# Optimization experiments

Hardware: AMD Instinct MI355X
Metric: run time of the kernel (lower is better)

The kernel has to match this reference:

```python
import jax, jax.numpy as jnp
import numpy as np

N_EMB = 1024
N_HEADS = 16
HS = N_EMB // N_HEADS  # 64
BASE = 10000.0


def _rope_cache(T):
    # theta uses dim = n_emb (as in the source), sliced to hs//2 frequencies
    i = jnp.arange(HS // 2, dtype=jnp.float32)
    theta = BASE ** (-2.0 * i / N_EMB)            # [hs/2]
    pos = jnp.arange(T, dtype=jnp.float32)        # [T]
    ang = pos[:, None] * theta[None, :]           # [T, hs/2]
    return jnp.cos(ang), jnp.sin(ang)


def _apply_rope(x, cos, sin):
    # x: [B, T, nh, hs]; rotate consecutive pairs along hs
    b, t, nh, hs = x.shape
    xr = x.reshape(b, t, nh, hs // 2, 2)
    c = cos[None, :, None, :]
    s = sin[None, :, None, :]
    r0 = xr[..., 0] * c - xr[..., 1] * s
    r1 = xr[..., 1] * c + xr[..., 0] * s
    return jnp.stack([r0, r1], axis=-1).reshape(b, t, nh, hs)


def setup_inputs() -> dict:
    key = jax.random.key(0)
    k1, k2, k3, k4 = jax.random.split(key, 4)
    B, T = 2, 2048
    w_std = 0.02
    x = jax.random.normal(k1, (B, T, N_EMB), jnp.float32)
    Wq = jax.random.normal(k2, (N_EMB, N_EMB), jnp.float32) * w_std
    Wk = jax.random.normal(k3, (N_EMB, N_EMB), jnp.float32) * w_std
    Wv = jax.random.normal(k4, (N_EMB, N_EMB), jnp.float32) * w_std
    return {"x": x, "Wq": Wq, "Wk": Wk, "Wv": Wv}


def reference(x, Wq, Wk, Wv):
    B, T, C = x.shape
    # nn.Linear(bias=False): y = x @ W.T
    q = (x @ Wq.T).reshape(B, T, N_HEADS, HS)
    k = (x @ Wk.T).reshape(B, T, N_HEADS, HS)
    v = (x @ Wv.T).reshape(B, T, N_HEADS, HS)
    cos, sin = _rope_cache(T)
    q = _apply_rope(q, cos, sin)
    k = _apply_rope(k, cos, sin)
    # scale uses C (n_emb), as in the source (not head_size)
    wei = jnp.einsum('bqhd,bkhd->bhqk', q, k) * (C ** -0.5)  # [B, nh, T, T]
    mask = jnp.tril(jnp.ones((T, T), dtype=bool))
    wei = jnp.where(mask[None, None], wei, -jnp.inf)
    wei = jax.nn.softmax(wei, axis=-1)
    # dropout is identity in eval mode
    out = jnp.einsum('bhqk,bkhd->bqhd', wei, v).reshape(B, T, C)
    return out
```

## Files before the change

kernel.cpp:

```cpp
#include <hip/hip_runtime.h>
#include <stdint.h>

typedef unsigned short u16;
typedef __bf16 bf16x8 __attribute__((ext_vector_type(8)));
typedef unsigned short u16x8 __attribute__((ext_vector_type(8)));
typedef unsigned short u16x4 __attribute__((ext_vector_type(4)));
typedef float f32x4 __attribute__((ext_vector_type(4)));
typedef uint32_t u32v4 __attribute__((ext_vector_type(4)));

#define LOG2E 1.4426950408889634f

typedef const __attribute__((address_space(1))) uint32_t as1_u32;
typedef __attribute__((address_space(3))) uint32_t as3_u32;

__device__ __forceinline__ u16 f2bf(float f) {
  union { float f; uint32_t i; } v; v.f = f;
  uint32_t r = (v.i + 0x7fffu + ((v.i >> 16) & 1u)) >> 16;
  return (u16)r;
}
__device__ __forceinline__ float bf2f(u16 u) {
  union { uint32_t i; float f; } v; v.i = ((uint32_t)u) << 16; return v.f;
}

__device__ __forceinline__ void gld_lds16(const void* g, void* l) {
  as1_u32* gp = (as1_u32*)((uintptr_t)g);
  as3_u32* lp = (as3_u32*)(uint32_t)(uintptr_t)(l);
  __builtin_amdgcn_global_load_lds(gp, lp, 16, 0, 0);
}

__device__ __forceinline__ float fast_exp2(float x) {
  float r;
  asm("v_exp_f32 %0, %1" : "=v"(r) : "v"(x));
  return r;
}

__global__ __launch_bounds__(256) void f32_to_bf16(
    const float* __restrict__ x, const float* __restrict__ wq,
    const float* __restrict__ wk, const float* __restrict__ wv,
    u16* __restrict__ xc, u16* __restrict__ wqc,
    u16* __restrict__ wkc, u16* __restrict__ wvc) {
  const int z = blockIdx.y;
  const float* src = z == 0 ? x : (z == 1 ? wq : (z == 2 ? wk : wv));
  u16* dst = z == 0 ? xc : (z == 1 ? wqc : (z == 2 ? wkc : wvc));
  const int n = z == 0 ? (1 << 22) : (1 << 20);

  const int idx = (blockIdx.x * 256 + (int)threadIdx.x) * 8;
  if (idx >= n) return;
  const f32x4 a = *(const f32x4*)&src[idx];
  const f32x4 b = *(const f32x4*)&src[idx + 4];
  u16x8 o;
#pragma unroll
  for (int j = 0; j < 4; j++) { o[j] = f2bf(a[j]); o[j + 4] = f2bf(b[j]); }
  *(u16x8*)&dst[idx] = o;
}

__global__ __launch_bounds__(256) void qkv_gemm(
    const u16* __restrict__ xc, const u16* __restrict__ wqc,
    const u16* __restrict__ wkc, const u16* __restrict__ wvc,
    u16* __restrict__ qo, u16* __restrict__ ko, u16* __restrict__ vt) {
  __shared__ __align__(16) u16 As[128 * 64];
  __shared__ __align__(16) u16 Bs[128 * 64];

  const int tid = threadIdx.x;
  const int lane = tid & 63;
  const int w = tid >> 6;
  const int wm = w >> 1, wn = w & 1;
  const int quad = lane >> 4, m16 = lane & 15;
  const int which = blockIdx.z;

  const u16* __restrict__ Ap;
  const u16* __restrict__ Bp;
  int m0, n0;
  if (which == 2) {
    Ap = wvc; Bp = xc;
    m0 = blockIdx.x * 128;
    n0 = blockIdx.y * 128;
  } else {
    Ap = xc; Bp = which == 0 ? wqc : wkc;
    m0 = blockIdx.y * 128;
    n0 = blockIdx.x * 128;
  }

  const f32x4 z4 = {0.f, 0.f, 0.f, 0.f};
  f32x4 acc[4][4];
#pragma unroll
  for (int i = 0; i < 4; i++)
#pragma unroll
    for (int j = 0; j < 4; j++) acc[i][j] = z4;

  const int lrow = lane >> 3;
  const int scol = ((lane & 7) ^ (lrow & 7)) * 8;
  const int srowA = m0 + w * 32 + lrow;
  const int srowB = n0 + w * 32 + lrow;
  const int rsw = m16 & 7;

  for (int k0 = 0; k0 < 1024; k0 += 64) {
    __syncthreads();
#pragma unroll
    for (int j = 0; j < 4; j++) {
      gld_lds16(&Ap[(size_t)(srowA + j * 8) * 1024 + k0 + scol],
                &As[(w * 32 + j * 8) * 64]);
      gld_lds16(&Bp[(size_t)(srowB + j * 8) * 1024 + k0 + scol],
                &Bs[(w * 32 + j * 8) * 64]);
    }
    __syncthreads();

#pragma unroll
    for (int kk = 0; kk < 2; kk++) {
      bf16x8 af[4], bfr[4];
      const int csw = ((kk * 4) ^ rsw) * 8;
#pragma unroll
      for (int t = 0; t < 4; t++) {
        af[t] = *(const bf16x8*)
            &As[(wm * 64 + t * 16 + m16) * 64 + (((kk * 4 + quad) ^ rsw) * 8)];
        bfr[t] = *(const bf16x8*)
            &Bs[(wn * 64 + t * 16 + m16) * 64 + (((kk * 4 + quad) ^ rsw) * 8)];
      }
      (void)csw;
#pragma unroll
      for (int mt = 0; mt < 4; mt++)
#pragma unroll
        for (int nt = 0; nt < 4; nt++)
          acc[mt][nt] = __builtin_amdgcn_mfma_f32_16x16x32_bf16(
              af[mt], bfr[nt], acc[mt][nt], 0, 0, 0);
    }
  }

  if (which < 2) {
    u16* __restrict__ out = which == 0 ? qo : ko;
#pragma unroll
    for (int mt = 0; mt < 4; mt++) {
      const int row = m0 + wm * 64 + mt * 16 + quad * 4;
#pragma unroll
      for (int nt = 0; nt < 4; nt++) {
        const int n = n0 + wn * 64 + nt * 16 + m16;
        f32x4 a = acc[mt][nt];
#pragma unroll
        for (int r = 0; r < 4; r++)
          out[(size_t)(row + r) * 1024 + n] = f2bf(a[r]);
      }
    }
  } else {
    const int m16p = (m16 & 3) | ((m16 & 4) << 1) | ((m16 & 8) >> 1);
#pragma unroll
    for (int mt = 0; mt < 4; mt++) {
      const int row = m0 + wm * 64 + mt * 16 + quad * 4;
#pragma unroll
      for (int nt = 0; nt < 4; nt++) {
        const int n = n0 + wn * 64 + nt * 16 + m16p;
        f32x4 a = acc[mt][nt];
#pragma unroll
        for (int r = 0; r < 4; r++)
          vt[(size_t)(row + r) * 4096 + n] = f2bf(a[r]);
      }
    }
  }
}

__global__ __launch_bounds__(256) void rope_inplace(u16* __restrict__ qb,
                                                    u16* __restrict__ kb) {
  u16* buf = blockIdx.y == 0 ? qb : kb;
  const int p = blockIdx.x * 256 + (int)threadIdx.x;
  const int e0 = p * 8;
  const int row = e0 >> 10;
  const int col0 = e0 & 1023;
  const int t = row & 2047;
  const float tf = (float)t;

  u16x8 d = *(const u16x8*)&buf[(size_t)row * 1024 + col0];
  u16x8 o;
#pragma unroll
  for (int j = 0; j < 4; j++) {
    const int i = ((col0 & 63) >> 1) + j;
    const float th = fast_exp2(-(float)i * 0.02595256324130752f);
    const float rev = tf * th * 0.15915494309189535f;
    float fr, s, c;
    asm("v_fract_f32 %0, %1" : "=v"(fr) : "v"(rev));
    asm("v_sin_f32 %0, %1" : "=v"(s) : "v"(fr));
    asm("v_cos_f32 %0, %1" : "=v"(c) : "v"(fr));
    const float a0 = bf2f(d[2 * j]), a1 = bf2f(d[2 * j + 1]);
    o[2 * j]     = f2bf(a0 * c - a1 * s);
    o[2 * j + 1] = f2bf(a1 * c + a0 * s);
  }
  *(u16x8*)&buf[(size_t)row * 1024 + col0] = o;
}

__global__ __launch_bounds__(256, 4) void flash_attn(
    const u16* __restrict__ qg, const u16* __restrict__ kg,
    const u16* __restrict__ vt, float* __restrict__ out) {
  __shared__ __align__(16) u16 Ks[128 * 72];
  __shared__ __align__(16) u16 Vs[64 * 136];

  const int tid = threadIdx.x, lane = tid & 63, w = tid >> 6;
  const int quad = lane >> 4, m16 = lane & 15;

  const int id   = (int)blockIdx.x;
  const int X    = id & 7;
  const int rem  = id >> 3;
  const int qt   = 31 - (rem >> 2);
  const int vloc = rem & 3;
  const int v    = X * 4 + vloc;
  const int h    = v & 15;
  const int b    = v >> 4;

  const size_t base  = (size_t)b * 2048 * 1024 + (size_t)h * 64;
  const size_t vbase = (size_t)(h * 64) * 4096 + (size_t)b * 2048;
  const float SC = 0.03125f * LOG2E;
  const f32x4 z4 = {0.f, 0.f, 0.f, 0.f};
  const int srow = tid >> 2, sc = (tid & 3) * 16;

  union { u16x8 u; bf16x8 f; } ones;
#pragma unroll
  for (int k = 0; k < 8; k++) ones.u[k] = 0x3F80;

  const int q0 = qt * 64;
  const int nr = (qt + 2) >> 1;

  const u16* qsrc = &qg[base + (size_t)(q0 + w * 16 + m16) * 1024 + quad * 8];
  const bf16x8 qf0 = *(const bf16x8*)qsrc;
  const bf16x8 qf1 = *(const bf16x8*)(qsrc + 32);

  u16x8 kr0, kr1, kr2, kr3, vr0, vr1, vr2, vr3;
  {
    const u16* ks = &kg[base + (size_t)srow * 1024 + sc];
    kr0 = *(const u16x8*)ks; kr1 = *(const u16x8*)(ks + 8);
    const u16* ks2 = ks + (size_t)64 * 1024;
    kr2 = *(const u16x8*)ks2; kr3 = *(const u16x8*)(ks2 + 8);
    const u16* vs = &vt[vbase + (size_t)srow * 4096 + sc];
    vr0 = *(const u16x8*)vs; vr1 = *(const u16x8*)(vs + 8);
    vr2 = *(const u16x8*)(vs + 64); vr3 = *(const u16x8*)(vs + 72);
  }

  f32x4 l4 = z4;
  f32x4 O[4];
#pragma unroll
  for (int d = 0; d < 4; d++) O[d] = z4;

  const int qrow0 = q0 + w * 16 + quad * 4;
  const int qcol  = q0 + w * 16 + m16;

  for (int rr = 0; rr < nr; ++rr) {
    const int k0 = rr * 128;
    if (rr) __syncthreads();
    *(u16x8*)&Ks[srow * 72 + sc] = kr0;
    *(u16x8*)&Ks[srow * 72 + sc + 8] = kr1;
    *(u16x8*)&Ks[(64 + srow) * 72 + sc] = kr2;
    *(u16x8*)&Ks[(64 + srow) * 72 + sc + 8] = kr3;
    *(u16x8*)&Vs[srow * 136 + sc] = vr0;
    *(u16x8*)&Vs[srow * 136 + sc + 8] = vr1;
    *(u16x8*)&Vs[srow * 136 + 64 + sc] = vr2;
    *(u16x8*)&Vs[srow * 136 + 64 + sc + 8] = vr3;
    __syncthreads();
    if (rr + 1 < nr) {
      const u16* ks = &kg[base + (size_t)(k0 + 128 + srow) * 1024 + sc];
      kr0 = *(const u16x8*)ks; kr1 = *(const u16x8*)(ks + 8);
      const u16* ks2 = ks + (size_t)64 * 1024;
      kr2 = *(const u16x8*)ks2; kr3 = *(const u16x8*)(ks2 + 8);
      const u16* vs = &vt[vbase + (size_t)srow * 4096 + k0 + 128 + sc];
      vr0 = *(const u16x8*)vs; vr1 = *(const u16x8*)(vs + 8);
      vr2 = *(const u16x8*)(vs + 64); vr3 = *(const u16x8*)(vs + 72);
    }

    f32x4 S[8];
#pragma unroll
    for (int nt = 0; nt < 8; nt++) {
      const bf16x8 kf0 = *(const bf16x8*)&Ks[(nt * 16 + m16) * 72 + quad * 8];
      const bf16x8 kf1 =
          *(const bf16x8*)&Ks[(nt * 16 + m16) * 72 + 32 + quad * 8];
      S[nt] = __builtin_amdgcn_mfma_f32_16x16x32_bf16(kf0, qf0, z4, 0, 0, 0);
      S[nt] = __builtin_amdgcn_mfma_f32_16x16x32_bf16(kf1, qf1, S[nt], 0, 0, 0);
    }

    const bool lastr = (rr == nr - 1);
    uint32_t W[16];
#pragma unroll
    for (int nt = 0; nt < 8; nt++) {
      float p[4];
#pragma unroll
      for (int r = 0; r < 4; r++) {
        float e = fast_exp2(S[nt][r] * SC);
        const int key = k0 + nt * 16 + quad * 4 + r;
        if (lastr && key > qcol) e = 0.f;
        p[r] = e;
      }
      uint32_t w0, w1;
      asm("v_cvt_pk_bf16_f32 %0, %1, %2" : "=v"(w0) : "v"(p[0]), "v"(p[1]));
      asm("v_cvt_pk_bf16_f32 %0, %1, %2" : "=v"(w1) : "v"(p[2]), "v"(p[3]));
      W[2 * nt] = w0; W[2 * nt + 1] = w1;
    }

    union { u32v4 u; bf16x8 f; } P[4];
#pragma unroll
    for (int ks = 0; ks < 4; ks++) {
      uint32_t a0 = W[4 * ks], b0 = W[4 * ks + 2];
      uint32_t a1 = W[4 * ks + 1], b1 = W[4 * ks + 3];
      asm("v_permlane32_swap_b32 %0, %1" : "+v"(a0), "+v"(b0));
      asm("v_permlane32_swap_b32 %0, %1" : "+v"(a1), "+v"(b1));
      P[ks].u = (u32v4){a0, a1, b0, b1};
    }

#pragma unroll
    for (int ks = 0; ks < 4; ks++)
      l4 = __builtin_amdgcn_mfma_f32_16x16x32_bf16(P[ks].f, ones.f, l4,
                                                   0, 0, 0);

#pragma unroll
    for (int dt = 0; dt < 4; dt++) {
#pragma unroll
      for (int ks = 0; ks < 4; ks++) {
        const bf16x8 vf =
            *(const bf16x8*)&Vs[(dt * 16 + m16) * 136 + ks * 32 + quad * 8];
        O[dt] = __builtin_amdgcn_mfma_f32_16x16x32_bf16(P[ks].f, vf, O[dt],
                                                        0, 0, 0);
      }
    }
  }

  float inv[4];
#pragma unroll
  for (int r = 0; r < 4; r++) inv[r] = 1.0f / l4[r];

#pragma unroll
  for (int dt = 0; dt < 4; dt++)
#pragma unroll
    for (int r = 0; r < 4; r++)
      out[base + (size_t)(qrow0 + r) * 1024 + dt * 16 + m16] =
          O[dt][r] * inv[r];
}

extern "C" void kernel_launch(void* const* d_in, const int* in_sizes, int n_in,
                              void* d_out, int out_size, void* d_ws, size_t ws_size,
                              hipStream_t stream) {
  const float* x  = (const float*)d_in[0];
  const float* Wq = (const float*)d_in[1];
  const float* Wk = (const float*)d_in[2];
  const float* Wv = (const float*)d_in[3];
  u16* qb  = (u16*)d_ws;
  u16* kb  = qb  + (size_t)4096 * 1024;
  u16* vtw = kb  + (size_t)4096 * 1024;
  u16* xc  = vtw + (size_t)4096 * 1024;
  u16* wqc = xc  + (size_t)4096 * 1024;
  u16* wkc = wqc + (size_t)1024 * 1024;
  u16* wvc = wkc + (size_t)1024 * 1024;

  f32_to_bf16<<<dim3(2048, 4), 256, 0, stream>>>(x, Wq, Wk, Wv,
                                                 xc, wqc, wkc, wvc);
  qkv_gemm<<<dim3(8, 32, 3), 256, 0, stream>>>(xc, wqc, wkc, wvc,
                                               qb, kb, vtw);
  rope_inplace<<<dim3(2048, 2), 256, 0, stream>>>(qb, kb);
  flash_attn<<<dim3(1024, 1, 1), 256, 0, stream>>>(qb, kb, vtw, (float*)d_out);
}
```

Before: 153.5 us.

## Fuse RoPE into QKV GEMM epilogue and process 128-row query tiles in attention

RoPE is now applied in the Q/K GEMM epilogue, rotating each pair with a lane-xor shuffle, so the separate in-place rope kernel and its extra read/write of Q and K are gone. The flash attention kernel now gives each wave two 16-row query groups (128 query rows per block). Each K/V tile loaded into LDS is reused twice as often, and the grid shrinks to 512 blocks with paired light/heavy causal tiles to balance load. The cost is higher register pressure, with launch bounds dropped to 2 blocks per SM, which lowers occupancy.

After: 162.0 us. +5.5%, slower.

```diff
diff --git a/kernel.cpp b/kernel.cpp
--- a/kernel.cpp
+++ b/kernel.cpp
@@ -4,7 +4,6 @@
 typedef unsigned short u16;
 typedef __bf16 bf16x8 __attribute__((ext_vector_type(8)));
 typedef unsigned short u16x8 __attribute__((ext_vector_type(8)));
-typedef unsigned short u16x4 __attribute__((ext_vector_type(4)));
 typedef float f32x4 __attribute__((ext_vector_type(4)));
 typedef uint32_t u32v4 __attribute__((ext_vector_type(4)));
 
@@ -108,7 +107,6 @@
 #pragma unroll
     for (int kk = 0; kk < 2; kk++) {
       bf16x8 af[4], bfr[4];
-      const int csw = ((kk * 4) ^ rsw) * 8;
 #pragma unroll
       for (int t = 0; t < 4; t++) {
         af[t] = *(const bf16x8*)
@@ -116,7 +114,6 @@
         bfr[t] = *(const bf16x8*)
             &Bs[(wn * 64 + t * 16 + m16) * 64 + (((kk * 4 + quad) ^ rsw) * 8)];
       }
-      (void)csw;
 #pragma unroll
       for (int mt = 0; mt < 4; mt++)
 #pragma unroll
@@ -128,6 +125,14 @@
 
   if (which < 2) {
     u16* __restrict__ out = which == 0 ? qo : ko;
+    float th[4];
+#pragma unroll
+    for (int nt = 0; nt < 4; nt++) {
+      const int i = ((nt * 16 + m16) & 63) >> 1;
+      th[nt] = fast_exp2(-(float)i * 0.02595256324130752f)
+               * 0.15915494309189535f;
+    }
+    const float sgn = (m16 & 1) ? 1.f : -1.f;
 #pragma unroll
     for (int mt = 0; mt < 4; mt++) {
       const int row = m0 + wm * 64 + mt * 16 + quad * 4;
@@ -136,8 +141,17 @@
         const int n = n0 + wn * 64 + nt * 16 + m16;
         f32x4 a = acc[mt][nt];
 #pragma unroll
-        for (int r = 0; r < 4; r++)
-          out[(size_t)(row + r) * 1024 + n] = f2bf(a[r]);
+        for (int r = 0; r < 4; r++) {
+          const int t = (row + r) & 2047;
+          const float rev = (float)t * th[nt];
+          float fr, sv, cv;
+          asm("v_fract_f32 %0, %1" : "=v"(fr) : "v"(rev));
+          asm("v_sin_f32 %0, %1" : "=v"(sv) : "v"(fr));
+          asm("v_cos_f32 %0, %1" : "=v"(cv) : "v"(fr));
+          const float own = a[r];
+          const float other = __shfl_xor(own, 1);
+          out[(size_t)(row + r) * 1024 + n] = f2bf(own * cv + other * (sgn * sv));
+        }
       }
     }
   } else {
@@ -157,35 +171,7 @@
   }
 }
 
-__global__ __launch_bounds__(256) void rope_inplace(u16* __restrict__ qb,
-                                                    u16* __restrict__ kb) {
-  u16* buf = blockIdx.y == 0 ? qb : kb;
-  const int p = blockIdx.x * 256 + (int)threadIdx.x;
-  const int e0 = p * 8;
-  const int row = e0 >> 10;
-  const int col0 = e0 & 1023;
-  const int t = row & 2047;
-  const float tf = (float)t;
-
-  u16x8 d = *(const u16x8*)&buf[(size_t)row * 1024 + col0];
-  u16x8 o;
-#pragma unroll
-  for (int j = 0; j < 4; j++) {
-    const int i = ((col0 & 63) >> 1) + j;
-    const float th = fast_exp2(-(float)i * 0.02595256324130752f);
-    const float rev = tf * th * 0.15915494309189535f;
-    float fr, s, c;
-    asm("v_fract_f32 %0, %1" : "=v"(fr) : "v"(rev));
-    asm("v_sin_f32 %0, %1" : "=v"(s) : "v"(fr));
-    asm("v_cos_f32 %0, %1" : "=v"(c) : "v"(fr));
-    const float a0 = bf2f(d[2 * j]), a1 = bf2f(d[2 * j + 1]);
-    o[2 * j]     = f2bf(a0 * c - a1 * s);
-    o[2 * j + 1] = f2bf(a1 * c + a0 * s);
-  }
-  *(u16x8*)&buf[(size_t)row * 1024 + col0] = o;
-}
-
-__global__ __launch_bounds__(256, 4) void flash_attn(
+__global__ __launch_bounds__(256, 2) void flash_attn(
     const u16* __restrict__ qg, const u16* __restrict__ kg,
     const u16* __restrict__ vt, float* __restrict__ out) {
   __shared__ __align__(16) u16 Ks[128 * 72];
@@ -197,8 +183,10 @@
   const int id   = (int)blockIdx.x;
   const int X    = id & 7;
   const int rem  = id >> 3;
-  const int qt   = 31 - (rem >> 2);
-  const int vloc = rem & 3;
+  const int s    = rem & 1;
+  const int vloc = (rem >> 1) & 3;
+  const int kk_  = rem >> 3;
+  const int Q    = s ? 15 - kk_ : kk_;
   const int v    = X * 4 + vloc;
   const int h    = v & 15;
   const int b    = v >> 4;
@@ -213,12 +201,15 @@
 #pragma unroll
   for (int k = 0; k < 8; k++) ones.u[k] = 0x3F80;
 
-  const int q0 = qt * 64;
-  const int nr = (qt + 2) >> 1;
-
-  const u16* qsrc = &qg[base + (size_t)(q0 + w * 16 + m16) * 1024 + quad * 8];
-  const bf16x8 qf0 = *(const bf16x8*)qsrc;
-  const bf16x8 qf1 = *(const bf16x8*)(qsrc + 32);
+  const int q0 = Q * 128;
+  const int nr = Q + 1;
+
+  const u16* qsA = &qg[base + (size_t)(q0 + w * 32 + m16) * 1024 + quad * 8];
+  const bf16x8 qfA0 = *(const bf16x8*)qsA;
+  const bf16x8 qfA1 = *(const bf16x8*)(qsA + 32);
+  const u16* qsB = qsA + (size_t)16 * 1024;
+  const bf16x8 qfB0 = *(const bf16x8*)qsB;
+  const bf16x8 qfB1 = *(const bf16x8*)(qsB + 32);
 
   u16x8 kr0, kr1, kr2, kr3, vr0, vr1, vr2, vr3;
   {
@@ -231,13 +222,13 @@
     vr2 = *(const u16x8*)(vs + 64); vr3 = *(const u16x8*)(vs + 72);
   }
 
-  f32x4 l4 = z4;
-  f32x4 O[4];
-#pragma unroll
-  for (int d = 0; d < 4; d++) O[d] = z4;
-
-  const int qrow0 = q0 + w * 16 + quad * 4;
-  const int qcol  = q0 + w * 16 + m16;
+  f32x4 lA = z4, lB = z4;
+  f32x4 OA[4], OB[4];
+#pragma unroll
+  for (int d = 0; d < 4; d++) { OA[d] = z4; OB[d] = z4; }
+
+  const int qrowA = q0 + w * 32 + quad * 4;
+  const int qcolA = q0 + w * 32 + m16;
 
   for (int rr = 0; rr < nr; ++rr) {
     const int k0 = rr * 128;
@@ -261,48 +252,80 @@
       vr2 = *(const u16x8*)(vs + 64); vr3 = *(const u16x8*)(vs + 72);
     }
 
-    f32x4 S[8];
+    f32x4 SA[8], SB[8];
 #pragma unroll
     for (int nt = 0; nt < 8; nt++) {
       const bf16x8 kf0 = *(const bf16x8*)&Ks[(nt * 16 + m16) * 72 + quad * 8];
       const bf16x8 kf1 =
           *(const bf16x8*)&Ks[(nt * 16 + m16) * 72 + 32 + quad * 8];
-      S[nt] = __builtin_amdgcn_mfma_f32_16x16x32_bf16(kf0, qf0, z4, 0, 0, 0);
-      S[nt] = __builtin_amdgcn_mfma_f32_16x16x32_bf16(kf1, qf1, S[nt], 0, 0, 0);
+      SA[nt] = __builtin_amdgcn_mfma_f32_16x16x32_bf16(kf0, qfA0, z4, 0, 0, 0);
+      SA[nt] = __builtin_amdgcn_mfma_f32_16x16x32_bf16(kf1, qfA1, SA[nt], 0, 0, 0);
+      SB[nt] = __builtin_amdgcn_mfma_f32_16x16x32_bf16(kf0, qfB0, z4, 0, 0, 0);
+      SB[nt] = __builtin_amdgcn_mfma_f32_16x16x32_bf16(kf1, qfB1, SB[nt], 0, 0, 0);
     }
 
     const bool lastr = (rr == nr - 1);
-    uint32_t W[16];
-#pragma unroll
-    for (int nt = 0; nt < 8; nt++) {
-      float p[4];
-#pragma unroll
-      for (int r = 0; r < 4; r++) {
-        float e = fast_exp2(S[nt][r] * SC);
-        const int key = k0 + nt * 16 + quad * 4 + r;
-        if (lastr && key > qcol) e = 0.f;
-        p[r] = e;
-      }
-      uint32_t w0, w1;
-      asm("v_cvt_pk_bf16_f32 %0, %1, %2" : "=v"(w0) : "v"(p[0]), "v"(p[1]));
-      asm("v_cvt_pk_bf16_f32 %0, %1, %2" : "=v"(w1) : "v"(p[2]), "v"(p[3]));
-      W[2 * nt] = w0; W[2 * nt + 1] = w1;
-    }
-
-    union { u32v4 u; bf16x8 f; } P[4];
+
+    union { u32v4 u; bf16x8 f; } PA[4], PB[4];
+    {
+      uint32_t W[16];
+#pragma unroll
+      for (int nt = 0; nt < 8; nt++) {
+        float p[4];
+#pragma unroll
+        for (int r = 0; r < 4; r++) {
+          float e = fast_exp2(SA[nt][r] * SC);
+          const int key = k0 + nt * 16 + quad * 4 + r;
+          if (lastr && key > qcolA) e = 0.f;
+          p[r] = e;
+        }
+        uint32_t w0, w1;
+        asm("v_cvt_pk_bf16_f32 %0, %1, %2" : "=v"(w0) : "v"(p[0]), "v"(p[1]));
+        asm("v_cvt_pk_bf16_f32 %0, %1, %2" : "=v"(w1) : "v"(p[2]), "v"(p[3]));
+        W[2 * nt] = w0; W[2 * nt + 1] = w1;
+      }
+#pragma unroll
+      for (int ks = 0; ks < 4; ks++) {
+        uint32_t a0 = W[4 * ks], b0 = W[4 * ks + 2];
+        uint32_t a1 = W[4 * ks + 1], b1 = W[4 * ks + 3];
+        asm("v_permlane32_swap_b32 %0, %1" : "+v"(a0), "+v"(b0));
+        asm("v_permlane32_swap_b32 %0, %1" : "+v"(a1), "+v"(b1));
+        PA[ks].u = (u32v4){a0, a1, b0, b1};
+      }
+    }
+    {
+      const int qcolB = qcolA + 16;
+      uint32_t W[16];
+#pragma unroll
+      for (int nt = 0; nt < 8; nt++) {
+        float p[4];
+#pragma unroll
+        for (int r = 0; r < 4; r++) {
+          float e = fast_exp2(SB[nt][r] * SC);
+          const int key = k0 + nt * 16 + quad * 4 + r;
+          if (lastr && key > qcolB) e = 0.f;
+          p[r] = e;
+        }
+        uint32_t w0, w1;
+        asm("v_cvt_pk_bf16_f32 %0, %1, %2" : "=v"(w0) : "v"(p[0]), "v"(p[1]));
+        asm("v_cvt_pk_bf16_f32 %0, %1, %2" : "=v"(w1) : "v"(p[2]), "v"(p[3]));
+        W[2 * nt] = w0; W[2 * nt + 1] = w1;
+      }
+#pragma unroll
+      for (int ks = 0; ks < 4; ks++) {
+        uint32_t a0 = W[4 * ks], b0 = W[4 * ks + 2];
+        uint32_t a1 = W[4 * ks + 1], b1 = W[4 * ks + 3];
+        asm("v_permlane32_swap_b32 %0, %1" : "+v"(a0), "+v"(b0));
+        asm("v_permlane32_swap_b32 %0, %1" : "+v"(a1), "+v"(b1));
+        PB[ks].u = (u32v4){a0, a1, b0, b1};
+      }
+    }
+
 #pragma unroll
     for (int ks = 0; ks < 4; ks++) {
-      uint32_t a0 = W[4 * ks], b0 = W[4 * ks + 2];
-      uint32_t a1 = W[4 * ks + 1], b1 = W[4 * ks + 3];
-      asm("v_permlane32_swap_b32 %0, %1" : "+v"(a0), "+v"(b0));
-      asm("v_permlane32_swap_b32 %0, %1" : "+v"(a1), "+v"(b1));
-      P[ks].u = (u32v4){a0, a1, b0, b1};
-    }
-
-#pragma unroll
-    for (int ks = 0; ks < 4; ks++)
-      l4 = __builtin_amdgcn_mfma_f32_16x16x32_bf16(P[ks].f, ones.f, l4,
-                                                   0, 0, 0);
+      lA = __builtin_amdgcn_mfma_f32_16x16x32_bf16(PA[ks].f, ones.f, lA, 0, 0, 0);
+      lB = __builtin_amdgcn_mfma_f32_16x16x32_bf16(PB[ks].f, ones.f, lB, 0, 0, 0);
+    }
 
 #pragma unroll
     for (int dt = 0; dt < 4; dt++) {
@@ -310,22 +333,27 @@
       for (int ks = 0; ks < 4; ks++) {
         const bf16x8 vf =
             *(const bf16x8*)&Vs[(dt * 16 + m16) * 136 + ks * 32 + quad * 8];
-        O[dt] = __builtin_amdgcn_mfma_f32_16x16x32_bf16(P[ks].f, vf, O[dt],
-                                                        0, 0, 0);
-      }
-    }
-  }
-
-  float inv[4];
-#pragma unroll
-  for (int r = 0; r < 4; r++) inv[r] = 1.0f / l4[r];
+        OA[dt] = __builtin_amdgcn_mfma_f32_16x16x32_bf16(PA[ks].f, vf, OA[dt],
+                                                         0, 0, 0);
+        OB[dt] = __builtin_amdgcn_mfma_f32_16x16x32_bf16(PB[ks].f, vf, OB[dt],
+                                                         0, 0, 0);
+      }
+    }
+  }
+
+  float invA[4], invB[4];
+#pragma unroll
+  for (int r = 0; r < 4; r++) { invA[r] = 1.0f / lA[r]; invB[r] = 1.0f / lB[r]; }
 
 #pragma unroll
   for (int dt = 0; dt < 4; dt++)
 #pragma unroll
-    for (int r = 0; r < 4; r++)
-      out[base + (size_t)(qrow0 + r) * 1024 + dt * 16 + m16] =
-          O[dt][r] * inv[r];
+    for (int r = 0; r < 4; r++) {
+      out[base + (size_t)(qrowA + r) * 1024 + dt * 16 + m16] =
+          OA[dt][r] * invA[r];
+      out[base + (size_t)(qrowA + 16 + r) * 1024 + dt * 16 + m16] =
+          OB[dt][r] * invB[r];
+    }
 }
 
 extern "C" void kernel_launch(void* const* d_in, const int* in_sizes, int n_in,
@@ -347,6 +375,5 @@
                                                  xc, wqc, wkc, wvc);
   qkv_gemm<<<dim3(8, 32, 3), 256, 0, stream>>>(xc, wqc, wkc, wvc,
                                                qb, kb, vtw);
-  rope_inplace<<<dim3(2048, 2), 256, 0, stream>>>(qb, kb);
-  flash_attn<<<dim3(1024, 1, 1), 256, 0, stream>>>(qb, kb, vtw, (float*)d_out);
-}
+  flash_attn<<<dim3(512, 1, 1), 256, 0, stream>>>(qb, kb, vtw, (float*)d_out);
+}
```
